# Kernel tuning notes

Measured on AMD Instinct MI355X. Metric: run time of the kernel, lower is better.

Reference implementation:

```python
import jax, jax.numpy as jnp
import numpy as np

N, B, D = 100000, 1024, 768  # total nodes, num graphs, feature dim
DE = 64                      # placeholder edge-feat dim (unused, passed through)


def setup_inputs() -> dict:
    key = jax.random.key(0)
    ks = jax.random.split(key, 6)
    feat = jax.random.normal(ks[0], (N, D), jnp.float32)
    vn_feat = jax.random.normal(ks[1], (B, D), jnp.float32)
    edge_feat = jax.random.normal(ks[2], (B, DE), jnp.float32)
    batch = jnp.sort(jax.random.randint(ks[3], (N,), 0, B)).astype(jnp.int32)
    fc_W = jax.random.normal(ks[4], (D, D), jnp.float32) * 0.02
    fc_b = jnp.zeros((D,), jnp.float32)
    proj_W = jax.random.normal(ks[5], (D, D), jnp.float32) * 0.02
    proj_b = jnp.zeros((D,), jnp.float32)
    return dict(feat=feat, vn_feat=vn_feat, edge_feat=edge_feat, batch=batch,
                num_graphs=B, fc_W=fc_W, fc_b=fc_b, proj_W=proj_W, proj_b=proj_b)


def _logsum_pool(feat, batch, num_graphs):
    # r_i = (log N_i / N_i) * sum_k x_k  == mean_pool * log(num_nodes)
    seg_sum = jax.ops.segment_sum(feat, batch, num_segments=num_graphs)  # [B, D]
    cnt = jax.ops.segment_sum(jnp.ones((feat.shape[0],), feat.dtype), batch,
                              num_segments=num_graphs)                   # [B]
    cnt = jnp.maximum(cnt, 1.0)  # guard empty graphs (torch would NaN)
    return (seg_sum / cnt[:, None]) * jnp.log(cnt)[:, None]


def reference(feat, vn_feat, edge_feat, batch, num_graphs, fc_W, fc_b, proj_W, proj_b):
    # 1) scatter-pool node features per graph (logsum pooling)
    pool = _logsum_pool(feat, batch, num_graphs)            # [B, D]
    # 2) FCLayer: Linear -> (norm=none) -> relu -> (dropout=0)
    h = jax.nn.relu((pool + vn_feat) @ fc_W + fc_b)         # [B, D]
    # 3) residual virtual-node update
    vn_new = vn_feat + h                                    # [B, D]
    # 4) project and broadcast-add back to every node
    feat_out = feat + (vn_new @ proj_W + proj_b)[batch]     # [N, D]
    # use_edges=False: edge features pass through unchanged
    return feat_out, vn_new, edge_feat
```

## Files before the change

### kernel.cpp

```cpp
#include <hip/hip_runtime.h>
#include <cmath>

#define THREADS 256
#define PCOLS 192

typedef __attribute__((ext_vector_type(8))) short bf16x8;
typedef __attribute__((ext_vector_type(4))) float f32x4;

__device__ __forceinline__ short f2bf(float f) {
    return (short)(__builtin_bit_cast(unsigned, f) >> 16);
}

typedef const __attribute__((address_space(1))) unsigned int* gas1_t;
typedef __attribute__((address_space(3))) unsigned int* las3_t;
__device__ __forceinline__ void gload16(const float* g, float* l) {
    __builtin_amdgcn_global_load_lds((gas1_t)g, (las3_t)l, 16, 0, 0);
}

__device__ __forceinline__ int lower_bound_i(const int* __restrict__ arr, int n, int val) {
    int lo = 0, hi = n;
    while (lo < hi) {
        int mid = (lo + hi) >> 1;
        if (arr[mid] < val) lo = mid + 1; else hi = mid;
    }
    return lo;
}

__device__ __forceinline__ float4 f4add(float4 a, float4 b) {
    a.x += b.x; a.y += b.y; a.z += b.z; a.w += b.w; return a;
}
__device__ __forceinline__ float4 f4fma(float4 a, float s, float4 b) {
    b.x += a.x * s; b.y += a.y * s; b.z += a.z * s; b.w += a.w * s; return b;
}

__global__ void pool_kernel(const float4* __restrict__ feat4, const float4* __restrict__ vn4,
                            const int* __restrict__ batch, float4* __restrict__ x4,
                            int N, int D4) {
    int g = blockIdx.x;
    __shared__ int s_range[2];
    if (threadIdx.x < 2) s_range[threadIdx.x] = lower_bound_i(batch, N, g + (int)threadIdx.x);
    __syncthreads();
    int lo = s_range[0], hi = s_range[1];
    int cnt = hi - lo;
    float scale = (cnt > 0) ? (logf((float)cnt) / (float)cnt) : 0.f;

    int t = threadIdx.x;
    float4 a0 = {0,0,0,0}, a1 = {0,0,0,0}, a2 = {0,0,0,0}, a3 = {0,0,0,0};
    float4 a4 = {0,0,0,0}, a5 = {0,0,0,0}, a6 = {0,0,0,0}, a7 = {0,0,0,0};

    const float4* __restrict__ p = feat4 + (size_t)lo * D4 + t;
    int r = lo;
    for (; r + 8 <= hi; r += 8) {
        float4 v0 = p[0 * (size_t)D4];
        float4 v1 = p[1 * (size_t)D4];
        float4 v2 = p[2 * (size_t)D4];
        float4 v3 = p[3 * (size_t)D4];
        float4 v4 = p[4 * (size_t)D4];
        float4 v5 = p[5 * (size_t)D4];
        float4 v6 = p[6 * (size_t)D4];
        float4 v7 = p[7 * (size_t)D4];
        a0 = f4add(a0, v0); a1 = f4add(a1, v1); a2 = f4add(a2, v2); a3 = f4add(a3, v3);
        a4 = f4add(a4, v4); a5 = f4add(a5, v5); a6 = f4add(a6, v6); a7 = f4add(a7, v7);
        p += 8 * (size_t)D4;
    }
    for (; r < hi; ++r) {
        a0 = f4add(a0, p[0]);
        p += D4;
    }
    float4 s = f4add(f4add(f4add(a0, a1), f4add(a2, a3)), f4add(f4add(a4, a5), f4add(a6, a7)));
    float4 vnv = vn4[(size_t)g * D4 + t];
    x4[(size_t)g * D4 + t] = f4fma(s, scale, vnv);
}

template <bool RELU, bool ADD_RES>
__global__ __launch_bounds__(256) void gemm_mfma(const float* __restrict__ A,
        const float* __restrict__ W, const float* __restrict__ bias,
        const float* __restrict__ res, float* __restrict__ out,
        int M, int Nn, int K) {
    __shared__ float lds[2][4096];
    const int tid = threadIdx.x;
    const int lane = tid & 63;
    const int wid = tid >> 6;
    const int wr = wid >> 1, wc = wid & 1;
    const int lrow = lane & 15;
    const int kg = lane >> 4;
    const int tileM = blockIdx.y * 64;
    const int tileN = blockIdx.x * 64;
    const int nk = K / 32;

    f32x4 acc[2][2] = {};

    #define STAGE(buf, kt) do {                                                   \
        float* Ld = lds[buf];                                                     \
        _Pragma("unroll")                                                         \
        for (int i = 0; i < 2; ++i) {                                             \
            int s = tid + i * 256;                                                \
            int row = s >> 3;                                                     \
            int c = (s & 7) ^ (row & 7);                                          \
            gload16(A + (size_t)(tileM + row) * K + (kt) * 32 + c * 4, Ld + s * 4); \
        }                                                                         \
        _Pragma("unroll")                                                         \
        for (int i = 0; i < 2; ++i) {                                             \
            int s = tid + i * 256;                                                \
            int k = s >> 4, n4 = s & 15;                                          \
            gload16(W + (size_t)((kt) * 32 + k) * Nn + tileN + n4 * 4,            \
                    Ld + 2048 + s * 4);                                           \
        }                                                                         \
    } while (0)

    STAGE(0, 0);
    __syncthreads();

    for (int kt = 0; kt < nk; ++kt) {
        if (kt + 1 < nk) STAGE((kt + 1) & 1, kt + 1);
        const float* As = lds[kt & 1];
        const float* Bs = As + 2048;
        bf16x8 a[2], b[2];
        #pragma unroll
        for (int m = 0; m < 2; ++m) {
            int row = wr * 32 + m * 16 + lrow;
            int c0 = (kg * 2) ^ (row & 7);
            int c1 = (kg * 2 + 1) ^ (row & 7);
            float4 f0 = *(const float4*)(As + (row * 8 + c0) * 4);
            float4 f1 = *(const float4*)(As + (row * 8 + c1) * 4);
            a[m][0] = f2bf(f0.x); a[m][1] = f2bf(f0.y);
            a[m][2] = f2bf(f0.z); a[m][3] = f2bf(f0.w);
            a[m][4] = f2bf(f1.x); a[m][5] = f2bf(f1.y);
            a[m][6] = f2bf(f1.z); a[m][7] = f2bf(f1.w);
        }
        #pragma unroll
        for (int n = 0; n < 2; ++n) {
            int col = wc * 32 + n * 16 + lrow;
            #pragma unroll
            for (int j = 0; j < 8; ++j)
                b[n][j] = f2bf(Bs[(kg * 8 + j) * 64 + col]);
        }
        #pragma unroll
        for (int m = 0; m < 2; ++m)
            #pragma unroll
            for (int n = 0; n < 2; ++n)
                acc[m][n] = __builtin_amdgcn_mfma_f32_16x16x32_bf16(a[m], b[n], acc[m][n], 0, 0, 0);
        __syncthreads();
    }

    #pragma unroll
    for (int m = 0; m < 2; ++m) {
        #pragma unroll
        for (int n = 0; n < 2; ++n) {
            int col = tileN + wc * 32 + n * 16 + lrow;
            float bv = bias[col];
            #pragma unroll
            for (int r = 0; r < 4; ++r) {
                int row = tileM + wr * 32 + m * 16 + kg * 4 + r;
                float v = acc[m][n][r] + bv;
                if (RELU) v = fmaxf(v, 0.f);
                if (ADD_RES) v += res[(size_t)row * Nn + col];
                out[(size_t)row * Nn + col] = v;
            }
        }
    }
    #undef STAGE
}

__global__ void node_add_kernel(const float4* __restrict__ feat4, const float4* __restrict__ y4,
                                const int* __restrict__ batch, float* __restrict__ out,
                                int N, int D4) {
    int node = N - 1 - (int)(blockIdx.x * blockDim.y + threadIdx.y);
    if (node < 0) return;
    int t = threadIdx.x;
    int b = batch[node];
    float4 f = feat4[(size_t)node * D4 + t];
    float4 v = y4[(size_t)b * D4 + t];
    f32x4 r;
    r.x = f.x + v.x; r.y = f.y + v.y; r.z = f.z + v.z; r.w = f.w + v.w;
    f32x4* dst = (f32x4*)(out + ((size_t)node * D4 + t) * 4);
    __builtin_nontemporal_store(r, dst);
}

extern "C" void kernel_launch(void* const* d_in, const int* in_sizes, int n_in,
                              void* d_out, int out_size, void* d_ws, size_t ws_size,
                              hipStream_t stream) {
    const float* feat  = (const float*)d_in[0];
    const float* vn    = (const float*)d_in[1];
    const float* edge  = (const float*)d_in[2];
    const int*   batch = (const int*)d_in[3];
    const float* fcW   = (const float*)d_in[5];
    const float* fcb   = (const float*)d_in[6];
    const float* pW    = (const float*)d_in[7];
    const float* pb    = (const float*)d_in[8];

    const int D = in_sizes[6];
    const int N = in_sizes[0] / D;
    const int B = in_sizes[1] / D;
    const int edge_elems = in_sizes[2];
    const int D4 = D / 4;

    float* out_feat = (float*)d_out;
    float* out_vn   = out_feat + (size_t)N * D;
    float* out_edge = out_vn + (size_t)B * D;

    float* x = (float*)d_ws;
    float* y = x + (size_t)B * D;

    pool_kernel<<<B, PCOLS, 0, stream>>>((const float4*)feat, (const float4*)vn,
                                         batch, (float4*)x, N, D4);

    dim3 gdim(D / 64, B / 64);
    gemm_mfma<true, true><<<gdim, THREADS, 0, stream>>>(x, fcW, fcb, vn, out_vn, B, D, D);

    gemm_mfma<false, false><<<gdim, THREADS, 0, stream>>>(out_vn, pW, pb, nullptr, y, B, D, D);

    dim3 nblk(192, 2);
    node_add_kernel<<<(N + 1) / 2, nblk, 0, stream>>>((const float4*)feat, (const float4*)y,
                                                      batch, out_feat, N, D4);

    hipMemcpyAsync(out_edge, edge, (size_t)edge_elems * sizeof(float),
                   hipMemcpyDeviceToDevice, stream);
}
```

Measured before the change: 206.5 us.

## Pre-convert GEMM operands to bf16 with transposed weights for vector LDS loads

Adds a kernel that converts both weight matrices to transposed bf16 each call. The pool kernel and first GEMM now write their activations as bf16. The GEMMs stage half-size bf16 tiles and read MFMA operands as single 16-byte LDS vectors, replacing scalar strided fp32 reads and per-element conversion. This costs an extra launch and redundant weight conversion on every call, but the GEMMs are a small part of a runtime dominated by memory-bound pooling and broadcast-add.

Result: faster. 188.3 us (-8.8%).

```diff
diff --git a/kernel.cpp b/kernel.cpp
--- a/kernel.cpp
+++ b/kernel.cpp
@@ -13,7 +13,7 @@
 
 typedef const __attribute__((address_space(1))) unsigned int* gas1_t;
 typedef __attribute__((address_space(3))) unsigned int* las3_t;
-__device__ __forceinline__ void gload16(const float* g, float* l) {
+__device__ __forceinline__ void gload16(const short* g, short* l) {
     __builtin_amdgcn_global_load_lds((gas1_t)g, (las3_t)l, 16, 0, 0);
 }
 
@@ -33,8 +33,25 @@
     b.x += a.x * s; b.y += a.y * s; b.z += a.z * s; b.w += a.w * s; return b;
 }
 
+__global__ void transpose_bf16(const float* __restrict__ src0, short* __restrict__ dst0,
+                               const float* __restrict__ src1, short* __restrict__ dst1,
+                               int n) {
+    const float* src = blockIdx.z ? src1 : src0;
+    short* dst = blockIdx.z ? dst1 : dst0;
+    __shared__ short tile[32][33];
+    int bx = blockIdx.x * 32, by = blockIdx.y * 32;
+    int tx = threadIdx.x, ty = threadIdx.y;
+    #pragma unroll
+    for (int i = 0; i < 32; i += 8)
+        tile[ty + i][tx] = f2bf(src[(size_t)(by + ty + i) * n + bx + tx]);
+    __syncthreads();
+    #pragma unroll
+    for (int i = 0; i < 32; i += 8)
+        dst[(size_t)(bx + ty + i) * n + by + tx] = tile[tx][ty + i];
+}
+
 __global__ void pool_kernel(const float4* __restrict__ feat4, const float4* __restrict__ vn4,
-                            const int* __restrict__ batch, float4* __restrict__ x4,
+                            const int* __restrict__ batch, short* __restrict__ xbf,
                             int N, int D4) {
     int g = blockIdx.x;
     __shared__ int s_range[2];
@@ -69,15 +86,18 @@
     }
     float4 s = f4add(f4add(f4add(a0, a1), f4add(a2, a3)), f4add(f4add(a4, a5), f4add(a6, a7)));
     float4 vnv = vn4[(size_t)g * D4 + t];
-    x4[(size_t)g * D4 + t] = f4fma(s, scale, vnv);
-}
-
-template <bool RELU, bool ADD_RES>
-__global__ __launch_bounds__(256) void gemm_mfma(const float* __restrict__ A,
-        const float* __restrict__ W, const float* __restrict__ bias,
+    float4 x = f4fma(s, scale, vnv);
+    short4 o;
+    o.x = f2bf(x.x); o.y = f2bf(x.y); o.z = f2bf(x.z); o.w = f2bf(x.w);
+    *(short4*)(xbf + ((size_t)g * D4 + t) * 4) = o;
+}
+
+template <bool RELU, bool ADD_RES, bool WRITE_BF>
+__global__ __launch_bounds__(256) void gemm_bf(const short* __restrict__ A,
+        const short* __restrict__ Wt, const float* __restrict__ bias,
         const float* __restrict__ res, float* __restrict__ out,
-        int M, int Nn, int K) {
-    __shared__ float lds[2][4096];
+        short* __restrict__ out_bf, int Nn, int K) {
+    __shared__ short lds[2][2][64 * 32];
     const int tid = threadIdx.x;
     const int lane = tid & 63;
     const int wid = tid >> 6;
@@ -90,50 +110,33 @@
 
     f32x4 acc[2][2] = {};
 
-    #define STAGE(buf, kt) do {                                                   \
-        float* Ld = lds[buf];                                                     \
-        _Pragma("unroll")                                                         \
-        for (int i = 0; i < 2; ++i) {                                             \
-            int s = tid + i * 256;                                                \
-            int row = s >> 3;                                                     \
-            int c = (s & 7) ^ (row & 7);                                          \
-            gload16(A + (size_t)(tileM + row) * K + (kt) * 32 + c * 4, Ld + s * 4); \
-        }                                                                         \
-        _Pragma("unroll")                                                         \
-        for (int i = 0; i < 2; ++i) {                                             \
-            int s = tid + i * 256;                                                \
-            int k = s >> 4, n4 = s & 15;                                          \
-            gload16(W + (size_t)((kt) * 32 + k) * Nn + tileN + n4 * 4,            \
-                    Ld + 2048 + s * 4);                                           \
-        }                                                                         \
+    const int srow = tid >> 2;
+    const int sci = (tid & 3) ^ (srow & 3);
+
+    #define STG(buf, kt) do {                                                    \
+        short* La = lds[buf][0];                                                 \
+        short* Lb = lds[buf][1];                                                 \
+        gload16(A  + (size_t)(tileM + srow) * K + (kt) * 32 + sci * 8, La + tid * 8); \
+        gload16(Wt + (size_t)(tileN + srow) * K + (kt) * 32 + sci * 8, Lb + tid * 8); \
     } while (0)
 
-    STAGE(0, 0);
+    STG(0, 0);
     __syncthreads();
 
     for (int kt = 0; kt < nk; ++kt) {
-        if (kt + 1 < nk) STAGE((kt + 1) & 1, kt + 1);
-        const float* As = lds[kt & 1];
-        const float* Bs = As + 2048;
+        if (kt + 1 < nk) STG((kt + 1) & 1, kt + 1);
+        const short* La = lds[kt & 1][0];
+        const short* Lb = lds[kt & 1][1];
         bf16x8 a[2], b[2];
         #pragma unroll
         for (int m = 0; m < 2; ++m) {
             int row = wr * 32 + m * 16 + lrow;
-            int c0 = (kg * 2) ^ (row & 7);
-            int c1 = (kg * 2 + 1) ^ (row & 7);
-            float4 f0 = *(const float4*)(As + (row * 8 + c0) * 4);
-            float4 f1 = *(const float4*)(As + (row * 8 + c1) * 4);
-            a[m][0] = f2bf(f0.x); a[m][1] = f2bf(f0.y);
-            a[m][2] = f2bf(f0.z); a[m][3] = f2bf(f0.w);
-            a[m][4] = f2bf(f1.x); a[m][5] = f2bf(f1.y);
-            a[m][6] = f2bf(f1.z); a[m][7] = f2bf(f1.w);
+            a[m] = *(const bf16x8*)(La + row * 32 + ((kg ^ (row & 3)) * 8));
         }
         #pragma unroll
         for (int n = 0; n < 2; ++n) {
             int col = wc * 32 + n * 16 + lrow;
-            #pragma unroll
-            for (int j = 0; j < 8; ++j)
-                b[n][j] = f2bf(Bs[(kg * 8 + j) * 64 + col]);
+            b[n] = *(const bf16x8*)(Lb + col * 32 + ((kg ^ (col & 3)) * 8));
         }
         #pragma unroll
         for (int m = 0; m < 2; ++m)
@@ -156,10 +159,11 @@
                 if (RELU) v = fmaxf(v, 0.f);
                 if (ADD_RES) v += res[(size_t)row * Nn + col];
                 out[(size_t)row * Nn + col] = v;
+                if (WRITE_BF) out_bf[(size_t)row * Nn + col] = f2bf(v);
             }
         }
     }
-    #undef STAGE
+    #undef STG
 }
 
 __global__ void node_add_kernel(const float4* __restrict__ feat4, const float4* __restrict__ y4,
@@ -199,16 +203,26 @@
     float* out_vn   = out_feat + (size_t)N * D;
     float* out_edge = out_vn + (size_t)B * D;
 
-    float* x = (float*)d_ws;
-    float* y = x + (size_t)B * D;
+    char* ws = (char*)d_ws;
+    short* xbf  = (short*)ws;
+    short* x2bf = (short*)(ws + (size_t)B * D * 2);
+    short* fcWt = (short*)(ws + (size_t)B * D * 4);
+    short* pWt  = (short*)(ws + (size_t)B * D * 4 + (size_t)D * D * 2);
+    float* y    = (float*)(ws + (size_t)B * D * 4 + (size_t)D * D * 4);
+
+    dim3 tb(32, 8);
+    dim3 tg(D / 32, D / 32, 2);
+    transpose_bf16<<<tg, tb, 0, stream>>>(fcW, fcWt, pW, pWt, D);
 
     pool_kernel<<<B, PCOLS, 0, stream>>>((const float4*)feat, (const float4*)vn,
-                                         batch, (float4*)x, N, D4);
+                                         batch, xbf, N, D4);
 
     dim3 gdim(D / 64, B / 64);
-    gemm_mfma<true, true><<<gdim, THREADS, 0, stream>>>(x, fcW, fcb, vn, out_vn, B, D, D);
-
-    gemm_mfma<false, false><<<gdim, THREADS, 0, stream>>>(out_vn, pW, pb, nullptr, y, B, D, D);
+    gemm_bf<true, true, true><<<gdim, THREADS, 0, stream>>>(xbf, fcWt, fcb, vn,
+                                                            out_vn, x2bf, D, D);
+
+    gemm_bf<false, false, false><<<gdim, THREADS, 0, stream>>>(x2bf, pWt, pb, nullptr,
+                                                               y, nullptr, D, D);
 
     dim3 nblk(192, 2);
     node_add_kernel<<<(N + 1) / 2, nblk, 0, stream>>>((const float4*)feat, (const float4*)y,
```
